# Kernel optimization log

Hardware: AMD Instinct MI355X
Metric: run time of the kernel (lower is better)

Reference implementation:

```python
import jax, jax.numpy as jnp
import numpy as np

D_MODEL = 128
N_HEADS = 4
HEAD_DIM = D_MODEL // N_HEADS


def setup_inputs() -> dict:
    key = jax.random.key(0)
    kx, kq, ko = jax.random.split(key, 3)
    B, T = 4, 4096
    x = jax.random.normal(kx, (B, T, D_MODEL), dtype=jnp.float32)
    s = 1.0 / np.sqrt(D_MODEL)
    # torch nn.Linear weight: [out, in]; y = x @ W.T
    W_qkv = jax.random.uniform(kq, (3 * D_MODEL, D_MODEL), dtype=jnp.float32, minval=-s, maxval=s)
    W_out = jax.random.uniform(ko, (D_MODEL, D_MODEL), dtype=jnp.float32, minval=-s, maxval=s)
    return {"x": x, "W_qkv": W_qkv, "W_out": W_out}


def reference(x, W_qkv, W_out):
    B, T, _ = x.shape
    qkv = (x @ W_qkv.T).reshape(B, T, 3, N_HEADS, HEAD_DIM)
    q, k, v = qkv[:, :, 0], qkv[:, :, 1], qkv[:, :, 2]  # [B,T,H,D]
    # scores: [B,H,T,T]
    scores = jnp.einsum('bthd,bshd->bhts', q, k) / jnp.sqrt(jnp.float32(HEAD_DIM))
    causal = jnp.triu(jnp.ones((T, T), dtype=bool), 1)
    scores = jnp.where(causal, -jnp.inf, scores)
    attn = jax.nn.softmax(scores, axis=-1)
    out = jnp.einsum('bhts,bshd->bthd', attn, v).reshape(B, T, D_MODEL)
    return out @ W_out.T
```

## Files before the change

### kernel.cpp

```cpp
#include <hip/hip_runtime.h>
#include <math.h>

#define B_   4
#define T_   4096
#define DM_  128
#define NH_  4
#define HD_  32
#define TOKENS (B_ * T_)

typedef __attribute__((ext_vector_type(8))) short short8;
typedef __attribute__((ext_vector_type(4))) float floatx4;

__device__ __forceinline__ unsigned short f2bf(float f) {
    union { float f; unsigned int u; } v; v.f = f;
    unsigned int u = v.u;
    u += 0x7fffu + ((u >> 16) & 1u);
    return (unsigned short)(u >> 16);
}
__device__ __forceinline__ void split_bf(float v, unsigned short& hi, unsigned short& lo) {
    unsigned short h = f2bf(v);
    float hf = __uint_as_float(((unsigned int)h) << 16);
    hi = h;
    lo = f2bf(v - hf);
}

#define LROW 136

__global__ __launch_bounds__(256) void qkv_proj_kernel(
    const float* __restrict__ x, const float* __restrict__ Wqkv,
    unsigned short* __restrict__ q_bf, unsigned short* __restrict__ k_bf,
    unsigned short* __restrict__ v_t)
{
    __shared__ __align__(16) unsigned short whi[64 * LROW];
    __shared__ __align__(16) unsigned short wlo[64 * LROW];

    const int tid  = threadIdx.x;
    const int wave = tid >> 6, lane = tid & 63;
    const int m    = lane & 15, q4 = lane >> 4;
    const int m0   = blockIdx.x * 64;
    const int ch   = blockIdx.y;
    const float scale = 0.2550052509571414f;

    {
        const float4* wg = (const float4*)(Wqkv + (size_t)ch * 64 * DM_);
        #pragma unroll
        for (int i = 0; i < 8; ++i) {
            const int f = tid + 256 * i;
            float4 v = wg[f];
            const int row = f >> 5, k4 = f & 31;
            ushort4 h, l;
            split_bf(v.x, h.x, l.x); split_bf(v.y, h.y, l.y);
            split_bf(v.z, h.z, l.z); split_bf(v.w, h.w, l.w);
            *(ushort4*)(whi + row * LROW + k4 * 4) = h;
            *(ushort4*)(wlo + row * LROW + k4 * 4) = l;
        }
    }

    short8 Ah[4], Al[4];
    {
        const float4* xg = (const float4*)(x + (size_t)(m0 + wave * 16 + m) * DM_);
        #pragma unroll
        for (int ks = 0; ks < 4; ++ks) {
            float4 a = xg[ks * 8 + q4 * 2];
            float4 b = xg[ks * 8 + q4 * 2 + 1];
            ushort4 h0, l0, h1, l1;
            split_bf(a.x, h0.x, l0.x); split_bf(a.y, h0.y, l0.y);
            split_bf(a.z, h0.z, l0.z); split_bf(a.w, h0.w, l0.w);
            split_bf(b.x, h1.x, l1.x); split_bf(b.y, h1.y, l1.y);
            split_bf(b.z, h1.z, l1.z); split_bf(b.w, h1.w, l1.w);
            Ah[ks] = short8{(short)h0.x, (short)h0.y, (short)h0.z, (short)h0.w,
                            (short)h1.x, (short)h1.y, (short)h1.z, (short)h1.w};
            Al[ks] = short8{(short)l0.x, (short)l0.y, (short)l0.z, (short)l0.w,
                            (short)l1.x, (short)l1.y, (short)l1.z, (short)l1.w};
        }
    }
    __syncthreads();

    #pragma unroll
    for (int nb = 0; nb < 4; ++nb) {
        floatx4 acc = {0.f, 0.f, 0.f, 0.f};
        #pragma unroll
        for (int ks = 0; ks < 4; ++ks) {
            short8 Bh = *(const short8*)(whi + (nb * 16 + m) * LROW + ks * 32 + q4 * 8);
            short8 Bl = *(const short8*)(wlo + (nb * 16 + m) * LROW + ks * 32 + q4 * 8);
            acc = __builtin_amdgcn_mfma_f32_16x16x32_bf16(Ah[ks], Bh, acc, 0, 0, 0);
            acc = __builtin_amdgcn_mfma_f32_16x16x32_bf16(Ah[ks], Bl, acc, 0, 0, 0);
            acc = __builtin_amdgcn_mfma_f32_16x16x32_bf16(Al[ks], Bh, acc, 0, 0, 0);
        }
        const int n    = ch * 64 + nb * 16 + m;
        const int cidx = n >> 7;
        const int hh   = (n >> 5) & 3;
        const int d    = n & 31;
        const int tok0 = m0 + wave * 16 + q4 * 4;
        const int b    = tok0 >> 12;
        const int t0   = tok0 & (T_ - 1);
        const int bh   = b * NH_ + hh;
        if (cidx == 0) {
            #pragma unroll
            for (int reg = 0; reg < 4; ++reg)
                q_bf[((size_t)bh * T_ + t0 + reg) * HD_ + d] = f2bf(acc[reg] * scale);
        } else if (cidx == 1) {
            #pragma unroll
            for (int reg = 0; reg < 4; ++reg)
                k_bf[((size_t)bh * T_ + t0 + reg) * HD_ + d] = f2bf(acc[reg]);
        } else {
            ushort4 p;
            p.x = f2bf(acc[0]); p.y = f2bf(acc[1]);
            p.z = f2bf(acc[2]); p.w = f2bf(acc[3]);
            *(ushort4*)(v_t + ((size_t)bh * HD_ + d) * T_ + t0) = p;
        }
    }
}

__global__ __launch_bounds__(256, 4) void attn_mfma_kernel(
    const unsigned short* __restrict__ qb, const unsigned short* __restrict__ kb,
    const unsigned short* __restrict__ vtb, float* __restrict__ og)
{
    __shared__ __align__(16) char smem[5120 + 4608 + 4 * 2304];
    char* kLds = smem;
    char* vLds = smem + 5120;
    const int tid  = threadIdx.x;
    const int wave = tid >> 6, lane = tid & 63;
    const int m    = lane & 15, q4 = lane >> 4;
    char* pT = smem + 9728 + wave * 2304;

    const int pid = blockIdx.x;
    const int xcd = pid & 7;
    const int r_  = pid >> 3;
    const int bh  = xcd * 2 + (r_ & 1);
    const int j_  = r_ >> 1;
    const int a_  = j_ & 15, k_ = j_ >> 4;
    const int qt  = (k_ == 0) ? a_ : (k_ == 1) ? 63 - a_
                  : (k_ == 2) ? 32 + a_ : 31 - a_;

    const size_t qkbase = (size_t)bh * T_ * HD_;
    const char* kg = (const char*)(kb + qkbase);
    const char* vg = (const char*)(vtb + qkbase);

    short8 qf = *(const short8*)((const char*)(qb + qkbase)
                 + (size_t)(qt * 64 + wave * 16 + m) * 64 + q4 * 16);
    const int qrow = wave * 16 + m;

    floatx4 O0 = {0.f, 0.f, 0.f, 0.f}, O1 = {0.f, 0.f, 0.f, 0.f};
    float mx = -INFINITY, ls = 0.f;

    for (int kt = 0; kt <= qt; ++kt) {
        __syncthreads();
        {
            const int krow = tid >> 2, ku = tid & 3;
            short8 kv = *(const short8*)(kg + (size_t)(kt * 64 + krow) * 64 + ku * 16);
            const int vd = tid >> 3, vu = tid & 7;
            short8 vv = *(const short8*)(vg + (size_t)vd * (T_ * 2)
                                            + (size_t)kt * 128 + vu * 16);
            *(short8*)(kLds + krow * 80 + ku * 16) = kv;
            *(short8*)(vLds + vd * 144 + vu * 16) = vv;
        }
        __syncthreads();

        floatx4 st[4];
        #pragma unroll
        for (int sb = 0; sb < 4; ++sb) {
            short8 kfrag = *(const short8*)(kLds + (sb * 16 + m) * 80 + q4 * 16);
            floatx4 z = {0.f, 0.f, 0.f, 0.f};
            st[sb] = __builtin_amdgcn_mfma_f32_16x16x32_bf16(kfrag, qf, z, 0, 0, 0);
        }

        if (kt == qt) {
            #pragma unroll
            for (int sb = 0; sb < 4; ++sb)
                #pragma unroll
                for (int reg = 0; reg < 4; ++reg)
                    if (sb * 16 + q4 * 4 + reg > qrow) st[sb][reg] = -INFINITY;
        }

        float rmax = -INFINITY;
        #pragma unroll
        for (int sb = 0; sb < 4; ++sb)
            #pragma unroll
            for (int reg = 0; reg < 4; ++reg) rmax = fmaxf(rmax, st[sb][reg]);
        rmax = fmaxf(rmax, __shfl_xor(rmax, 16, 64));
        rmax = fmaxf(rmax, __shfl_xor(rmax, 32, 64));

        const float mn = fmaxf(mx, rmax);
        const float alpha = __builtin_amdgcn_exp2f(mx - mn);
        mx = mn;

        float psum = 0.f;
        #pragma unroll
        for (int sb = 0; sb < 4; ++sb) {
            float p0 = __builtin_amdgcn_exp2f(st[sb][0] - mn);
            float p1 = __builtin_amdgcn_exp2f(st[sb][1] - mn);
            float p2 = __builtin_amdgcn_exp2f(st[sb][2] - mn);
            float p3 = __builtin_amdgcn_exp2f(st[sb][3] - mn);
            psum += (p0 + p1) + (p2 + p3);
            unsigned u0 = __float_as_uint(p0) + 0x8000u;
            unsigned u1 = __float_as_uint(p1) + 0x8000u;
            unsigned u2 = __float_as_uint(p2) + 0x8000u;
            unsigned u3 = __float_as_uint(p3) + 0x8000u;
            uint2 pk;
            pk.x = __builtin_amdgcn_perm(u1, u0, 0x07060302);
            pk.y = __builtin_amdgcn_perm(u3, u2, 0x07060302);
            *(uint2*)(pT + m * 144 + sb * 32 + q4 * 8) = pk;
        }
        psum += __shfl_xor(psum, 16, 64);
        psum += __shfl_xor(psum, 32, 64);
        ls = ls * alpha + psum;
        #pragma unroll
        for (int reg = 0; reg < 4; ++reg) { O0[reg] *= alpha; O1[reg] *= alpha; }

        __asm__ volatile("s_waitcnt lgkmcnt(0)" ::: "memory");

        short8 b0  = *(const short8*)(pT + m * 144 + q4 * 16);
        short8 b1  = *(const short8*)(pT + m * 144 + 64 + q4 * 16);
        short8 v00 = *(const short8*)(vLds + m * 144 + q4 * 16);
        short8 v10 = *(const short8*)(vLds + m * 144 + 64 + q4 * 16);
        short8 v01 = *(const short8*)(vLds + (16 + m) * 144 + q4 * 16);
        short8 v11 = *(const short8*)(vLds + (16 + m) * 144 + 64 + q4 * 16);
        O0 = __builtin_amdgcn_mfma_f32_16x16x32_bf16(v00, b0, O0, 0, 0, 0);
        O0 = __builtin_amdgcn_mfma_f32_16x16x32_bf16(v10, b1, O0, 0, 0, 0);
        O1 = __builtin_amdgcn_mfma_f32_16x16x32_bf16(v01, b0, O1, 0, 0, 0);
        O1 = __builtin_amdgcn_mfma_f32_16x16x32_bf16(v11, b1, O1, 0, 0, 0);
    }

    const float inv = 1.f / ls;
    const int b = bh >> 2, h = bh & 3;
    const int t = qt * 64 + qrow;
    float* orow = og + (((size_t)b * T_ + t) * NH_ + h) * HD_;
    *(float4*)(orow + q4 * 4)      = make_float4(O0[0] * inv, O0[1] * inv,
                                                 O0[2] * inv, O0[3] * inv);
    *(float4*)(orow + 16 + q4 * 4) = make_float4(O1[0] * inv, O1[1] * inv,
                                                 O1[2] * inv, O1[3] * inv);
}

__global__ __launch_bounds__(256) void out_proj_kernel(
    const float* __restrict__ a, const float* __restrict__ Wout,
    float* __restrict__ out)
{
    __shared__ __align__(16) unsigned short whi[64 * LROW];
    __shared__ __align__(16) unsigned short wlo[64 * LROW];

    const int tid  = threadIdx.x;
    const int wave = tid >> 6, lane = tid & 63;
    const int m    = lane & 15, q4 = lane >> 4;
    const int m0   = blockIdx.x * 64;
    const int ch   = blockIdx.y;

    {
        const float4* wg = (const float4*)(Wout + (size_t)ch * 64 * DM_);
        #pragma unroll
        for (int i = 0; i < 8; ++i) {
            const int f = tid + 256 * i;
            float4 v = wg[f];
            const int row = f >> 5, k4 = f & 31;
            ushort4 h, l;
            split_bf(v.x, h.x, l.x); split_bf(v.y, h.y, l.y);
            split_bf(v.z, h.z, l.z); split_bf(v.w, h.w, l.w);
            *(ushort4*)(whi + row * LROW + k4 * 4) = h;
            *(ushort4*)(wlo + row * LROW + k4 * 4) = l;
        }
    }

    short8 Ah[4], Al[4];
    {
        const float4* xg = (const float4*)(a + (size_t)(m0 + wave * 16 + m) * DM_);
        #pragma unroll
        for (int ks = 0; ks < 4; ++ks) {
            float4 av = xg[ks * 8 + q4 * 2];
            float4 bv = xg[ks * 8 + q4 * 2 + 1];
            ushort4 h0, l0, h1, l1;
            split_bf(av.x, h0.x, l0.x); split_bf(av.y, h0.y, l0.y);
            split_bf(av.z, h0.z, l0.z); split_bf(av.w, h0.w, l0.w);
            split_bf(bv.x, h1.x, l1.x); split_bf(bv.y, h1.y, l1.y);
            split_bf(bv.z, h1.z, l1.z); split_bf(bv.w, h1.w, l1.w);
            Ah[ks] = short8{(short)h0.x, (short)h0.y, (short)h0.z, (short)h0.w,
                            (short)h1.x, (short)h1.y, (short)h1.z, (short)h1.w};
            Al[ks] = short8{(short)l0.x, (short)l0.y, (short)l0.z, (short)l0.w,
                            (short)l1.x, (short)l1.y, (short)l1.z, (short)l1.w};
        }
    }
    __syncthreads();

    #pragma unroll
    for (int nb = 0; nb < 4; ++nb) {
        floatx4 acc = {0.f, 0.f, 0.f, 0.f};
        #pragma unroll
        for (int ks = 0; ks < 4; ++ks) {
            short8 Bh = *(const short8*)(whi + (nb * 16 + m) * LROW + ks * 32 + q4 * 8);
            short8 Bl = *(const short8*)(wlo + (nb * 16 + m) * LROW + ks * 32 + q4 * 8);
            acc = __builtin_amdgcn_mfma_f32_16x16x32_bf16(Ah[ks], Bh, acc, 0, 0, 0);
            acc = __builtin_amdgcn_mfma_f32_16x16x32_bf16(Ah[ks], Bl, acc, 0, 0, 0);
            acc = __builtin_amdgcn_mfma_f32_16x16x32_bf16(Al[ks], Bh, acc, 0, 0, 0);
        }
        const int n = ch * 64 + nb * 16 + m;
        const int tok0 = m0 + wave * 16 + q4 * 4;
        #pragma unroll
        for (int reg = 0; reg < 4; ++reg)
            out[(size_t)(tok0 + reg) * DM_ + n] = acc[reg];
    }
}

extern "C" void kernel_launch(void* const* d_in, const int* in_sizes, int n_in,
                              void* d_out, int out_size, void* d_ws, size_t ws_size,
                              hipStream_t stream) {
    const float* x    = (const float*)d_in[0];
    const float* Wqkv = (const float*)d_in[1];
    const float* Wout = (const float*)d_in[2];
    float* out = (float*)d_out;

    char* ws = (char*)d_ws;
    unsigned short* q_bf  = (unsigned short*)(ws);
    unsigned short* k_bf  = (unsigned short*)(ws + (size_t)4 * 1024 * 1024);
    unsigned short* v_t   = (unsigned short*)(ws + (size_t)8 * 1024 * 1024);
    float*          att_ws = (float*)(ws + (size_t)12 * 1024 * 1024);

    qkv_proj_kernel<<<dim3(TOKENS / 64, 6), 256, 0, stream>>>(x, Wqkv, q_bf, k_bf, v_t);
    attn_mfma_kernel<<<1024, 256, 0, stream>>>(q_bf, k_bf, v_t, att_ws);
    out_proj_kernel<<<dim3(TOKENS / 64, 2), 256, 0, stream>>>(att_ws, Wout, out);
}
```

Before: 147.9 us.

## Load K/V fragments directly from global into registers, drop shared staging and barriers

The attention kernel no longer stages K and V tiles through LDS with two block barriers per iteration. Each wave now loads its MFMA K fragments straight from global memory, prefetching the next tile's K into registers, and loads its V fragments directly. The per-wave P transpose buffer uses an XOR-swizzled 128-byte row layout instead of padding. This removes barriers and LDS traffic but makes each wave fetch K/V redundantly from global/L2, four times per block, and adds register pressure.

```diff
diff --git a/kernel.cpp b/kernel.cpp
--- a/kernel.cpp
+++ b/kernel.cpp
@@ -116,13 +116,12 @@
     const unsigned short* __restrict__ qb, const unsigned short* __restrict__ kb,
     const unsigned short* __restrict__ vtb, float* __restrict__ og)
 {
-    __shared__ __align__(16) char smem[5120 + 4608 + 4 * 2304];
-    char* kLds = smem;
-    char* vLds = smem + 5120;
+    __shared__ __align__(16) char smem[4 * 2048];
     const int tid  = threadIdx.x;
     const int wave = tid >> 6, lane = tid & 63;
     const int m    = lane & 15, q4 = lane >> 4;
-    char* pT = smem + 9728 + wave * 2304;
+    char* pT = smem + wave * 2048 + m * 128;
+    const int msw = m & 7;
 
     const int pid = blockIdx.x;
     const int xcd = pid & 7;
@@ -141,28 +140,35 @@
                  + (size_t)(qt * 64 + wave * 16 + m) * 64 + q4 * 16);
     const int qrow = wave * 16 + m;
 
+    const char* kp  = kg + (size_t)m * 64 + q4 * 16;
+    const char* vp0 = vg + (size_t)m * (T_ * 2) + q4 * 16;
+    const char* vp1 = vg + (size_t)(16 + m) * (T_ * 2) + q4 * 16;
+
     floatx4 O0 = {0.f, 0.f, 0.f, 0.f}, O1 = {0.f, 0.f, 0.f, 0.f};
     float mx = -INFINITY, ls = 0.f;
 
+    short8 kf[4];
+    #pragma unroll
+    for (int sb = 0; sb < 4; ++sb)
+        kf[sb] = *(const short8*)(kp + sb * 1024);
+
     for (int kt = 0; kt <= qt; ++kt) {
-        __syncthreads();
-        {
-            const int krow = tid >> 2, ku = tid & 3;
-            short8 kv = *(const short8*)(kg + (size_t)(kt * 64 + krow) * 64 + ku * 16);
-            const int vd = tid >> 3, vu = tid & 7;
-            short8 vv = *(const short8*)(vg + (size_t)vd * (T_ * 2)
-                                            + (size_t)kt * 128 + vu * 16);
-            *(short8*)(kLds + krow * 80 + ku * 16) = kv;
-            *(short8*)(vLds + vd * 144 + vu * 16) = vv;
-        }
-        __syncthreads();
-
         floatx4 st[4];
         #pragma unroll
         for (int sb = 0; sb < 4; ++sb) {
-            short8 kfrag = *(const short8*)(kLds + (sb * 16 + m) * 80 + q4 * 16);
             floatx4 z = {0.f, 0.f, 0.f, 0.f};
-            st[sb] = __builtin_amdgcn_mfma_f32_16x16x32_bf16(kfrag, qf, z, 0, 0, 0);
+            st[sb] = __builtin_amdgcn_mfma_f32_16x16x32_bf16(kf[sb], qf, z, 0, 0, 0);
+        }
+
+        short8 v00 = *(const short8*)(vp0 + kt * 128);
+        short8 v10 = *(const short8*)(vp0 + kt * 128 + 64);
+        short8 v01 = *(const short8*)(vp1 + kt * 128);
+        short8 v11 = *(const short8*)(vp1 + kt * 128 + 64);
+
+        if (kt < qt) {
+            #pragma unroll
+            for (int sb = 0; sb < 4; ++sb)
+                kf[sb] = *(const short8*)(kp + (size_t)(kt + 1) * 4096 + sb * 1024);
         }
 
         if (kt == qt) {
@@ -200,7 +206,7 @@
             uint2 pk;
             pk.x = __builtin_amdgcn_perm(u1, u0, 0x07060302);
             pk.y = __builtin_amdgcn_perm(u3, u2, 0x07060302);
-            *(uint2*)(pT + m * 144 + sb * 32 + q4 * 8) = pk;
+            *(uint2*)(pT + ((((2 * sb + (q4 >> 1)) ^ msw) << 4) + (q4 & 1) * 8)) = pk;
         }
         psum += __shfl_xor(psum, 16, 64);
         psum += __shfl_xor(psum, 32, 64);
@@ -210,12 +216,8 @@
 
         __asm__ volatile("s_waitcnt lgkmcnt(0)" ::: "memory");
 
-        short8 b0  = *(const short8*)(pT + m * 144 + q4 * 16);
-        short8 b1  = *(const short8*)(pT + m * 144 + 64 + q4 * 16);
-        short8 v00 = *(const short8*)(vLds + m * 144 + q4 * 16);
-        short8 v10 = *(const short8*)(vLds + m * 144 + 64 + q4 * 16);
-        short8 v01 = *(const short8*)(vLds + (16 + m) * 144 + q4 * 16);
-        short8 v11 = *(const short8*)(vLds + (16 + m) * 144 + 64 + q4 * 16);
+        short8 b0 = *(const short8*)(pT + ((q4 ^ msw) << 4));
+        short8 b1 = *(const short8*)(pT + (((q4 + 4) ^ msw) << 4));
         O0 = __builtin_amdgcn_mfma_f32_16x16x32_bf16(v00, b0, O0, 0, 0, 0);
         O0 = __builtin_amdgcn_mfma_f32_16x16x32_bf16(v10, b1, O0, 0, 0, 0);
         O1 = __builtin_amdgcn_mfma_f32_16x16x32_bf16(v01, b0, O1, 0, 0, 0);
```

After: 170.3 us. 1.15x slower.

## Process 128-key tiles per iteration in causal attention kernel

Applied to the files above, without the earlier changes.

The attention loop now stages 128 keys per iteration instead of 64, which halves the number of block barriers and online-softmax rescale steps. A templated helper handles the final partial tile with causal masking. The P staging buffer moves to an XOR-swizzled layout to reduce LDS bank conflicts. Shared memory roughly doubles (about 35KB per block), which may limit occupancy at the requested 4 blocks per CU, and register pressure rises with 8 score fragments.

```diff
diff --git a/kernel.cpp b/kernel.cpp
--- a/kernel.cpp
+++ b/kernel.cpp
@@ -112,17 +112,98 @@
     }
 }
 
+template<bool LAST>
+__device__ __forceinline__ void attn_tile128(
+    const char* kLds, const char* vLds, char* pT,
+    const int m, const int q4, const short8 qf,
+    const int sbN_in, const int limit,
+    floatx4& O0, floatx4& O1, float& mx, float& ls)
+{
+    const int sbN = LAST ? sbN_in : 8;
+    const int kN  = sbN >> 1;
+
+    floatx4 st[8];
+    #pragma unroll
+    for (int sb = 0; sb < 8; ++sb) {
+        if (sb >= sbN) continue;
+        short8 kfrag = *(const short8*)(kLds + (sb * 16 + m) * 80 + q4 * 16);
+        floatx4 z = {0.f, 0.f, 0.f, 0.f};
+        st[sb] = __builtin_amdgcn_mfma_f32_16x16x32_bf16(kfrag, qf, z, 0, 0, 0);
+    }
+
+    if (LAST) {
+        #pragma unroll
+        for (int sb = 0; sb < 8; ++sb) {
+            if (sb >= sbN) continue;
+            #pragma unroll
+            for (int reg = 0; reg < 4; ++reg)
+                if (sb * 16 + q4 * 4 + reg > limit) st[sb][reg] = -INFINITY;
+        }
+    }
+
+    float fm[8];
+    #pragma unroll
+    for (int sb = 0; sb < 8; ++sb)
+        fm[sb] = (sb < sbN) ? fmaxf(fmaxf(st[sb][0], st[sb][1]),
+                                    fmaxf(st[sb][2], st[sb][3]))
+                            : -INFINITY;
+    float rmax = fmaxf(fmaxf(fmaxf(fm[0], fm[1]), fmaxf(fm[2], fm[3])),
+                       fmaxf(fmaxf(fm[4], fm[5]), fmaxf(fm[6], fm[7])));
+    rmax = fmaxf(rmax, __shfl_xor(rmax, 16, 64));
+    rmax = fmaxf(rmax, __shfl_xor(rmax, 32, 64));
+
+    const float mn = fmaxf(mx, rmax);
+    const float alpha = __builtin_amdgcn_exp2f(mx - mn);
+    mx = mn;
+
+    float psum = 0.f;
+    #pragma unroll
+    for (int sb = 0; sb < 8; ++sb) {
+        if (sb >= sbN) continue;
+        float p0 = __builtin_amdgcn_exp2f(st[sb][0] - mn);
+        float p1 = __builtin_amdgcn_exp2f(st[sb][1] - mn);
+        float p2 = __builtin_amdgcn_exp2f(st[sb][2] - mn);
+        float p3 = __builtin_amdgcn_exp2f(st[sb][3] - mn);
+        psum += (p0 + p1) + (p2 + p3);
+        unsigned u0 = __float_as_uint(p0) + 0x8000u;
+        unsigned u1 = __float_as_uint(p1) + 0x8000u;
+        unsigned u2 = __float_as_uint(p2) + 0x8000u;
+        unsigned u3 = __float_as_uint(p3) + 0x8000u;
+        uint2 pk;
+        pk.x = __builtin_amdgcn_perm(u1, u0, 0x07060302);
+        pk.y = __builtin_amdgcn_perm(u3, u2, 0x07060302);
+        *(uint2*)(pT + ((((2 * sb + (q4 >> 1)) ^ m) << 4) + (q4 & 1) * 8)) = pk;
+    }
+    psum += __shfl_xor(psum, 16, 64);
+    psum += __shfl_xor(psum, 32, 64);
+    ls = ls * alpha + psum;
+    #pragma unroll
+    for (int reg = 0; reg < 4; ++reg) { O0[reg] *= alpha; O1[reg] *= alpha; }
+
+    __asm__ volatile("s_waitcnt lgkmcnt(0)" ::: "memory");
+
+    #pragma unroll
+    for (int ks = 0; ks < 4; ++ks) {
+        if (ks >= kN) continue;
+        short8 bfrag = *(const short8*)(pT + (((ks * 4 + q4) ^ m) << 4));
+        short8 va = *(const short8*)(vLds + m * 272 + ks * 64 + q4 * 16);
+        short8 vb = *(const short8*)(vLds + (16 + m) * 272 + ks * 64 + q4 * 16);
+        O0 = __builtin_amdgcn_mfma_f32_16x16x32_bf16(va, bfrag, O0, 0, 0, 0);
+        O1 = __builtin_amdgcn_mfma_f32_16x16x32_bf16(vb, bfrag, O1, 0, 0, 0);
+    }
+}
+
 __global__ __launch_bounds__(256, 4) void attn_mfma_kernel(
     const unsigned short* __restrict__ qb, const unsigned short* __restrict__ kb,
     const unsigned short* __restrict__ vtb, float* __restrict__ og)
 {
-    __shared__ __align__(16) char smem[5120 + 4608 + 4 * 2304];
+    __shared__ __align__(16) char smem[10240 + 8704 + 4 * 4096];
     char* kLds = smem;
-    char* vLds = smem + 5120;
+    char* vLds = smem + 10240;
     const int tid  = threadIdx.x;
     const int wave = tid >> 6, lane = tid & 63;
     const int m    = lane & 15, q4 = lane >> 4;
-    char* pT = smem + 9728 + wave * 2304;
+    char* pT = smem + 18944 + wave * 4096 + m * 256;
 
     const int pid = blockIdx.x;
     const int xcd = pid & 7;
@@ -144,82 +225,34 @@
     floatx4 O0 = {0.f, 0.f, 0.f, 0.f}, O1 = {0.f, 0.f, 0.f, 0.f};
     float mx = -INFINITY, ls = 0.f;
 
-    for (int kt = 0; kt <= qt; ++kt) {
+    const int itN      = (qt >> 1) + 1;
+    const int sbN_last = (qt & 1) ? 8 : 4;
+    const int limit    = ((qt & 1) << 6) + qrow;
+
+    for (int it = 0; it < itN; ++it) {
+        const int base = it << 7;
         __syncthreads();
         {
             const int krow = tid >> 2, ku = tid & 3;
-            short8 kv = *(const short8*)(kg + (size_t)(kt * 64 + krow) * 64 + ku * 16);
+            const char* ksrc = kg + (size_t)(base + krow) * 64 + ku * 16;
+            short8 k0 = *(const short8*)(ksrc);
+            short8 k1 = *(const short8*)(ksrc + 64 * 64);
             const int vd = tid >> 3, vu = tid & 7;
-            short8 vv = *(const short8*)(vg + (size_t)vd * (T_ * 2)
-                                            + (size_t)kt * 128 + vu * 16);
-            *(short8*)(kLds + krow * 80 + ku * 16) = kv;
-            *(short8*)(vLds + vd * 144 + vu * 16) = vv;
+            const char* vsrc = vg + (size_t)vd * (T_ * 2) + (size_t)base * 2 + vu * 16;
+            short8 vv0 = *(const short8*)(vsrc);
+            short8 vv1 = *(const short8*)(vsrc + 128);
+            *(short8*)(kLds + krow * 80 + ku * 16) = k0;
+            *(short8*)(kLds + (64 + krow) * 80 + ku * 16) = k1;
+            *(short8*)(vLds + vd * 272 + vu * 16) = vv0;
+            *(short8*)(vLds + vd * 272 + 128 + vu * 16) = vv1;
         }
         __syncthreads();
 
-        floatx4 st[4];
-        #pragma unroll
-        for (int sb = 0; sb < 4; ++sb) {
-            short8 kfrag = *(const short8*)(kLds + (sb * 16 + m) * 80 + q4 * 16);
-            floatx4 z = {0.f, 0.f, 0.f, 0.f};
-            st[sb] = __builtin_amdgcn_mfma_f32_16x16x32_bf16(kfrag, qf, z, 0, 0, 0);
-        }
-
-        if (kt == qt) {
-            #pragma unroll
-            for (int sb = 0; sb < 4; ++sb)
-                #pragma unroll
-                for (int reg = 0; reg < 4; ++reg)
-                    if (sb * 16 + q4 * 4 + reg > qrow) st[sb][reg] = -INFINITY;
-        }
-
-        float rmax = -INFINITY;
-        #pragma unroll
-        for (int sb = 0; sb < 4; ++sb)
-            #pragma unroll
-            for (int reg = 0; reg < 4; ++reg) rmax = fmaxf(rmax, st[sb][reg]);
-        rmax = fmaxf(rmax, __shfl_xor(rmax, 16, 64));
-        rmax = fmaxf(rmax, __shfl_xor(rmax, 32, 64));
-
-        const float mn = fmaxf(mx, rmax);
-        const float alpha = __builtin_amdgcn_exp2f(mx - mn);
-        mx = mn;
-
-        float psum = 0.f;
-        #pragma unroll
-        for (int sb = 0; sb < 4; ++sb) {
-            float p0 = __builtin_amdgcn_exp2f(st[sb][0] - mn);
-            float p1 = __builtin_amdgcn_exp2f(st[sb][1] - mn);
-            float p2 = __builtin_amdgcn_exp2f(st[sb][2] - mn);
-            float p3 = __builtin_amdgcn_exp2f(st[sb][3] - mn);
-            psum += (p0 + p1) + (p2 + p3);
-            unsigned u0 = __float_as_uint(p0) + 0x8000u;
-            unsigned u1 = __float_as_uint(p1) + 0x8000u;
-            unsigned u2 = __float_as_uint(p2) + 0x8000u;
-            unsigned u3 = __float_as_uint(p3) + 0x8000u;
-            uint2 pk;
-            pk.x = __builtin_amdgcn_perm(u1, u0, 0x07060302);
-            pk.y = __builtin_amdgcn_perm(u3, u2, 0x07060302);
-            *(uint2*)(pT + m * 144 + sb * 32 + q4 * 8) = pk;
-        }
-        psum += __shfl_xor(psum, 16, 64);
-        psum += __shfl_xor(psum, 32, 64);
-        ls = ls * alpha + psum;
-        #pragma unroll
-        for (int reg = 0; reg < 4; ++reg) { O0[reg] *= alpha; O1[reg] *= alpha; }
-
-        __asm__ volatile("s_waitcnt lgkmcnt(0)" ::: "memory");
-
-        short8 b0  = *(const short8*)(pT + m * 144 + q4 * 16);
-        short8 b1  = *(const short8*)(pT + m * 144 + 64 + q4 * 16);
-        short8 v00 = *(const short8*)(vLds + m * 144 + q4 * 16);
-        short8 v10 = *(const short8*)(vLds + m * 144 + 64 + q4 * 16);
-        short8 v01 = *(const short8*)(vLds + (16 + m) * 144 + q4 * 16);
-        short8 v11 = *(const short8*)(vLds + (16 + m) * 144 + 64 + q4 * 16);
-        O0 = __builtin_amdgcn_mfma_f32_16x16x32_bf16(v00, b0, O0, 0, 0, 0);
-        O0 = __builtin_amdgcn_mfma_f32_16x16x32_bf16(v10, b1, O0, 0, 0, 0);
-        O1 = __builtin_amdgcn_mfma_f32_16x16x32_bf16(v01, b0, O1, 0, 0, 0);
-        O1 = __builtin_amdgcn_mfma_f32_16x16x32_bf16(v11, b1, O1, 0, 0, 0);
+        if (it + 1 < itN)
+            attn_tile128<false>(kLds, vLds, pT, m, q4, qf, 8, 0, O0, O1, mx, ls);
+        else
+            attn_tile128<true>(kLds, vLds, pT, m, q4, qf, sbN_last, limit,
+                               O0, O1, mx, ls);
     }
 
     const float inv = 1.f / ls;
```

Result: faster. 135.4 us (-8.5%).
